# Performance work log

Measured on AMD Instinct MI355X. Metric: run time of the kernel, lower is better.

Reference implementation:

```python
import jax, jax.numpy as jnp
import numpy as np

BS = 256          # batch_size
NN = BS - 1
D = 128           # projection dim
SIGMA = 0.07      # rbf gamma (self.sigma)
C = 1.0
REG = 0.1
NUM_ITERS = 1000
ETA = 0.001
USE_NORM = True


def setup_inputs() -> dict:
    key = jax.random.key(0)
    k1, k2 = jax.random.split(key)
    z = jax.random.normal(k1, (BS, 2, D), dtype=jnp.float32)
    alpha_init = jax.random.normal(k2, (BS, NN, 1), dtype=jnp.float32)
    return {"z": z, "alpha_init": alpha_init}


def _rbf_kernel(X, Y, gamma):
    # exp(-gamma * ||x - y||^2)
    xn = jnp.sum(X * X, axis=1, keepdims=True)          # [n,1]
    yn = jnp.sum(Y * Y, axis=1, keepdims=True).T        # [1,m]
    d = xn + yn - 2.0 * (X @ Y.T)
    return jnp.exp(-gamma * d)


def _pgd_nesterov(DD, p, alpha0, eta, num_iters, C, use_norm):
    # minimize 0.5 a'DDa - p'a  s.t. 0 <= a <= C, batched over bs
    def step(carry, t):
        alpha, alpha_prev = carry
        beta = t / (t + 3.0)
        y = alpha + beta * (alpha - alpha_prev)
        grad = jnp.einsum('bij,bjk->bik', DD, y) - p     # [bs,nn,1]
        if use_norm:
            grad = grad / (jnp.linalg.norm(grad, axis=1, keepdims=True) + 1e-12)
        alpha_new = jnp.clip(y - eta * grad, 0.0, C)
        return (alpha_new, alpha), None
    (alpha, _), _ = jax.lax.scan(step, (alpha0, alpha0),
                                 jnp.arange(num_iters, dtype=jnp.float32))
    return alpha


def reference(z, alpha_init):
    bs, nn = BS, NN
    # F.normalize(z, p=2, dim=1): normalize over the view axis (faithful to source)
    nrm = jnp.maximum(jnp.linalg.norm(z, axis=1, keepdims=True), 1e-12)
    ftr = z / nrm
    ftr = jnp.concatenate([ftr[:, 0, :], ftr[:, 1, :]], axis=0)   # [2bs, d]

    K = _rbf_kernel(ftr[:bs], ftr, SIGMA)                          # [bs, 2bs]

    # ---- QP construction + solve under no_grad ----
    Kd = jax.lax.stop_gradient(K)
    KK = Kd[:, :bs]                                                # block: first bs cols
    r = jnp.arange(bs)
    m = jnp.arange(nn)
    # idx[i] = [0..bs-1] without i  (KMASK row/col removal)
    idx = m[None, :] + (m[None, :] >= r[:, None]).astype(jnp.int32)  # [bs, nn]
    KK_sub = KK[idx[:, :, None], idx[:, None, :]]                  # [bs,nn,nn]
    row = jnp.take_along_axis(KK, idx, axis=1)                     # row[i,m]=KK[i,idx[i,m]]
    # Delta[i,j,k] = 1 + reg*d_jk + KK[j,k] - KK[i,j] - KK[i,k]  (j,k != i)
    DD = (1.0 + REG * jnp.eye(nn, dtype=KK.dtype)[None]
          + KK_sub - row[:, :, None] - row[:, None, :])            # [bs,nn,nn]

    p = 2.0 * jnp.ones((bs, nn, 1), dtype=jnp.float32)
    alpha0 = jnp.clip(jax.nn.relu(alpha_init), 0.0, C)
    alpha = _pgd_nesterov(DD, p, alpha0, ETA, NUM_ITERS, C, USE_NORM)
    alpha_y = jnp.clip(jax.nn.relu(alpha[:, :, 0]), 0.0, C)
    alpha_y = jax.lax.stop_gradient(alpha_y)                       # [bs,nn]
    alpha_x = alpha_y.sum(axis=1)                                  # [bs]

    # ---- loss terms (grad flows through K here) ----
    Ks = K[:, bs:]                                                 # block12: [bs,bs]
    # Kn.T[i,m] = Ks.T[i, idx[i,m]]  (neg_mask = off-diagonal)
    KnT = jnp.take_along_axis(Ks.T, idx, axis=1)                   # [bs,nn]
    pos = jnp.diagonal(Ks)                                         # pos_mask = eye
    pos_loss = jnp.mean(alpha_x * pos)
    neg_loss = jnp.sum(alpha_y * KnT) / bs
    loss = neg_loss - pos_loss

    sparsity = ((alpha_y == C).sum().astype(jnp.float32)
                / ((alpha_y > 0).sum().astype(jnp.float32) + 1e-10))
    num_zero = (alpha_y == 0.0).mean()
    return (loss, pos.mean(), KnT.mean(), sparsity, num_zero, jnp.float32(0.0))
```

## Files before the change

### kernel.cpp

```cpp
#include <hip/hip_runtime.h>
#include <math.h>

#define BS   256
#define NN   255
#define DIM  128
#define GAMMA 0.07
#define NUM_ITERS 1000

typedef float v2f __attribute__((ext_vector_type(2)));

__device__ __forceinline__ double wred_d(double v) {
  #pragma unroll
  for (int k = 1; k < 64; k <<= 1) v += __shfl_xor(v, k, 64);
  return v;
}
__device__ __forceinline__ int wred_i(int v) {
  #pragma unroll
  for (int k = 1; k < 64; k <<= 1) v += __shfl_xor(v, k, 64);
  return v;
}

__device__ __forceinline__ float RLF(float v, int lane) {
  return __int_as_float(__builtin_amdgcn_readlane(__float_as_int(v), lane));
}

template <int CTRL, int RMASK>
__device__ __forceinline__ float dpp_add(float x) {
  int t = __builtin_amdgcn_update_dpp(0, __float_as_int(x), CTRL, RMASK, 0xf, true);
  return x + __int_as_float(t);
}
__device__ __forceinline__ float wred64_dpp(float x) {
  x = dpp_add<0x111, 0xf>(x);
  x = dpp_add<0x112, 0xf>(x);
  x = dpp_add<0x114, 0xf>(x);
  x = dpp_add<0x118, 0xf>(x);
  x = dpp_add<0x142, 0xa>(x);
  x = dpp_add<0x143, 0xc>(x);
  return RLF(x, 63);
}

__device__ __forceinline__ float rsq_nr(float x) {
  float r;
  asm("v_rsq_f32 %0, %1" : "=v"(r) : "v"(x));
  r = r * (1.5f - 0.5f * x * r * r);
  return r;
}

__device__ __forceinline__ void pk_fma(v2f& acc, const v2f& k, const v2f& y) {
  asm("v_pk_fma_f32 %0, %1, %2, %0" : "+v"(acc) : "v"(k), "v"(y));
}

__device__ __forceinline__ v2f pk_add(v2f a, v2f b) {
  v2f d;
  asm("v_pk_add_f32 %0, %1, %2" : "=v"(d) : "v"(a), "v"(b));
  return d;
}

__global__ void k_ftr(const float* __restrict__ z, double* __restrict__ ftrT) {
  int b = blockIdx.x;
  int d = threadIdx.x;
  double z0 = (double)z[b * 256 + d];
  double z1 = (double)z[b * 256 + 128 + d];
  double n = sqrt(z0 * z0 + z1 * z1);
  n = fmax(n, 1e-12);
  ftrT[d * 512 + b]       = z0 / n;
  ftrT[d * 512 + 256 + b] = z1 / n;
}

__global__ void k_K(const double* __restrict__ ftrT, float* __restrict__ K,
                    double* __restrict__ pk_knt, double* __restrict__ pos_arr) {
  int i = blockIdx.x;
  int t = threadIdx.x;
  __shared__ double rowi[DIM];
  __shared__ double redd[4];
  if (t < DIM) rowi[t] = ftrT[t * 512 + i];
  __syncthreads();
  double xn = 0.0;
  #pragma unroll 8
  for (int d = 0; d < DIM; ++d) xn += rowi[d] * rowi[d];

  double knt_part = 0.0;
  #pragma unroll
  for (int h = 0; h < 2; ++h) {
    int j = t + h * 256;
    double dot = 0.0, sq = 0.0;
    #pragma unroll 8
    for (int d = 0; d < DIM; ++d) {
      double f = ftrT[d * 512 + j];
      dot += rowi[d] * f;
      sq  += f * f;
    }
    double dist = xn + sq - 2.0 * dot;
    double kv = exp(-GAMMA * dist);
    K[i * 512 + j] = (float)kv;
    if (h == 1) {
      if (j == 256 + i) pos_arr[i] = kv;
      else knt_part += kv;
    }
  }
  double w = wred_d(knt_part);
  if ((t & 63) == 0) redd[t >> 6] = w;
  __syncthreads();
  if (t == 0) pk_knt[i] = redd[0] + redd[1] + redd[2] + redd[3];
}

__global__ __launch_bounds__(512, 2) void k_pgd(
    const float* __restrict__ K, const float* __restrict__ alpha_init,
    double* __restrict__ neg_arr, double* __restrict__ sa_arr,
    int* __restrict__ cnt1, int* __restrict__ cntp, int* __restrict__ cnt0) {
  int r = blockIdx.x;
  int tid = threadIdx.x;
  int l = tid & 63;
  int rg = tid >> 6;

  __shared__ __align__(16) float ytil[BS];
  __shared__ __align__(16) float part[8][BS];
  __shared__ float betat[1024];

  for (int i = tid; i < 1024; i += 512)
    betat[i] = (float)i / ((float)i + 3.0f);

  v2f kq[64];
  #pragma unroll
  for (int j = 0; j < 16; ++j) {
    float4 r0 = *(const float4*)&K[(32 * rg + 2 * j + 0) * 512 + 4 * l];
    float4 r1 = *(const float4*)&K[(32 * rg + 2 * j + 1) * 512 + 4 * l];
    kq[j].x      = r0.x; kq[j].y      = r1.x;
    kq[16 + j].x = r0.y; kq[16 + j].y = r1.y;
    kq[32 + j].x = r0.z; kq[32 + j].y = r1.z;
    kq[48 + j].x = r0.w; kq[48 + j].y = r1.w;
  }
  #pragma unroll
  for (int j = 0; j < 64; ++j)
    asm volatile("" : "+v"(kq[j]));

  float al[4], ap[4], yv[4], kv[4], rm2[4];
  if (rg == 0) {
    #pragma unroll
    for (int k = 0; k < 4; ++k) {
      int a = 4 * l + k;
      if (a == r) {
        al[k] = 0.f; ap[k] = 0.f; yv[k] = 0.f; kv[k] = 0.f; rm2[k] = 0.f;
      } else {
        int c = a - (a > r ? 1 : 0);
        float v = alpha_init[r * NN + c];
        v = fminf(fmaxf(v, 0.f), 1.f);
        al[k] = v; ap[k] = v; yv[k] = v;
        kv[k] = 1.0f - K[r * 512 + a];
        rm2[k] = 2.0f;
      }
    }
    float4 y4 = {yv[0], yv[1], yv[2], yv[3]};
    *(float4*)&ytil[4 * l] = y4;
  }
  __syncthreads();

  int rq = r >> 2, rc = r & 3;

  for (int it = 0; it < NUM_ITERS; ++it) {
    float beta;
    if (rg == 0) beta = betat[it + 1];

    const float4* yb = (const float4*)&ytil[32 * rg];
    v2f a0 = {0.f, 0.f}, a1 = {0.f, 0.f}, a2 = {0.f, 0.f}, a3 = {0.f, 0.f};
    #pragma unroll
    for (int jj = 0; jj < 8; ++jj) {
      float4 yq = yb[jj];
      v2f ylo = {yq.x, yq.y};
      v2f yhi = {yq.z, yq.w};
      pk_fma(a0, kq[2 * jj],      ylo); pk_fma(a0, kq[2 * jj + 1],      yhi);
      pk_fma(a1, kq[16 + 2 * jj], ylo); pk_fma(a1, kq[16 + 2 * jj + 1], yhi);
      pk_fma(a2, kq[32 + 2 * jj], ylo); pk_fma(a2, kq[32 + 2 * jj + 1], yhi);
      pk_fma(a3, kq[48 + 2 * jj], ylo); pk_fma(a3, kq[48 + 2 * jj + 1], yhi);
    }
    float4 accw = {a0.x + a0.y, a1.x + a1.y, a2.x + a2.y, a3.x + a3.y};

    float Sv;
    if (rg != 0) {
      *(float4*)&part[rg][4 * l] = accw;
    } else {
      Sv = wred64_dpp((yv[0] + yv[1]) + (yv[2] + yv[3]));
    }
    __syncthreads();

    if (rg == 0) {
      v2f q0l = {accw.x, accw.y}, q0h = {accw.z, accw.w};
      float4 q1 = *(const float4*)&part[1][4 * l];
      float4 q2 = *(const float4*)&part[2][4 * l];
      float4 q3 = *(const float4*)&part[3][4 * l];
      float4 q4 = *(const float4*)&part[4][4 * l];
      float4 q5 = *(const float4*)&part[5][4 * l];
      float4 q6 = *(const float4*)&part[6][4 * l];
      float4 q7 = *(const float4*)&part[7][4 * l];
      v2f s01l = pk_add(q0l, (v2f){q1.x, q1.y});
      v2f s01h = pk_add(q0h, (v2f){q1.z, q1.w});
      v2f s23l = pk_add((v2f){q2.x, q2.y}, (v2f){q3.x, q3.y});
      v2f s23h = pk_add((v2f){q2.z, q2.w}, (v2f){q3.z, q3.w});
      v2f s45l = pk_add((v2f){q4.x, q4.y}, (v2f){q5.x, q5.y});
      v2f s45h = pk_add((v2f){q4.z, q4.w}, (v2f){q5.z, q5.w});
      v2f s67l = pk_add((v2f){q6.x, q6.y}, (v2f){q7.x, q7.y});
      v2f s67h = pk_add((v2f){q6.z, q6.w}, (v2f){q7.z, q7.w});
      v2f sAl = pk_add(s01l, s23l);
      v2f sAh = pk_add(s01h, s23h);
      v2f sBl = pk_add(s45l, s67l);
      v2f sBh = pk_add(s45h, s67h);
      v2f gAl = pk_add(sAl, sBl);
      v2f gAh = pk_add(sAh, sBh);
      float4 gA = {gAl.x, gAl.y, gAh.x, gAh.y};
      float grv = (rc == 0) ? gA.x : (rc == 1) ? gA.y : (rc == 2) ? gA.z : gA.w;
      float gr = RLF(grv, rq);
      float g[4];
      g[0] = (gA.x - gr) - rm2[0] + kv[0] * Sv + 0.1f * yv[0];
      g[1] = (gA.y - gr) - rm2[1] + kv[1] * Sv + 0.1f * yv[1];
      g[2] = (gA.z - gr) - rm2[2] + kv[2] * Sv + 0.1f * yv[2];
      g[3] = (gA.w - gr) - rm2[3] + kv[3] * Sv + 0.1f * yv[3];
      float n2 = wred64_dpp((g[0] * g[0] + g[1] * g[1]) + (g[2] * g[2] + g[3] * g[3]));
      float sinv = 0.001f * rsq_nr(n2);
      #pragma unroll
      for (int k = 0; k < 4; ++k) {
        float na = fminf(fmaxf(fmaf(-sinv, g[k], yv[k]), 0.f), 1.f);
        ap[k] = al[k];
        al[k] = na;
        yv[k] = fmaf(beta, na - ap[k], na);
      }
      float4 y4 = {yv[0], yv[1], yv[2], yv[3]};
      *(float4*)&ytil[4 * l] = y4;
    }
    __syncthreads();
  }

  if (rg == 0) {
    double nl = 0.0, sa = 0.0;
    int c1 = 0, cp = 0, cz = 0;
    #pragma unroll
    for (int k = 0; k < 4; ++k) {
      int a = 4 * l + k;
      if (a != r) {
        float kx = K[a * 512 + 256 + r];
        nl += (double)al[k] * (double)kx;
        sa += (double)al[k];
        c1 += (al[k] == 1.0f);
        cp += (al[k] > 0.0f);
        cz += (al[k] == 0.0f);
      }
    }
    nl = wred_d(nl); sa = wred_d(sa);
    c1 = wred_i(c1); cp = wred_i(cp); cz = wred_i(cz);
    if (l == 0) {
      neg_arr[r] = nl;
      sa_arr[r]  = sa;
      cnt1[r] = c1; cntp[r] = cp; cnt0[r] = cz;
    }
  }
}

__global__ void k_fin(const double* __restrict__ pk_knt, const double* __restrict__ pos_arr,
                      const double* __restrict__ neg_arr, const double* __restrict__ sa_arr,
                      const int* __restrict__ cnt1, const int* __restrict__ cntp,
                      const int* __restrict__ cnt0, float* __restrict__ out) {
  int t = threadIdx.x;
  __shared__ double rd[16];
  __shared__ int ri[12];
  double knt = pk_knt[t];
  double pos = pos_arr[t];
  double neg = neg_arr[t];
  double pl  = sa_arr[t] * pos_arr[t];
  int a1 = cnt1[t], ap = cntp[t], a0 = cnt0[t];
  knt = wred_d(knt); pos = wred_d(pos); neg = wred_d(neg); pl = wred_d(pl);
  a1 = wred_i(a1); ap = wred_i(ap); a0 = wred_i(a0);
  int w = t >> 6;
  if ((t & 63) == 0) {
    rd[w] = knt; rd[4 + w] = pos; rd[8 + w] = neg; rd[12 + w] = pl;
    ri[w] = a1; ri[4 + w] = ap; ri[8 + w] = a0;
  }
  __syncthreads();
  if (t == 0) {
    double kntS = rd[0] + rd[1] + rd[2] + rd[3];
    double posS = rd[4] + rd[5] + rd[6] + rd[7];
    double negS = rd[8] + rd[9] + rd[10] + rd[11];
    double plS  = rd[12] + rd[13] + rd[14] + rd[15];
    int c1t = ri[0] + ri[1] + ri[2] + ri[3];
    int cpt = ri[4] + ri[5] + ri[6] + ri[7];
    int c0t = ri[8] + ri[9] + ri[10] + ri[11];
    out[0] = (float)(negS / 256.0 - plS / 256.0);
    out[1] = (float)(posS / 256.0);
    out[2] = (float)(kntS / (256.0 * 255.0));
    out[3] = (float)c1t / ((float)cpt + 1e-10f);
    out[4] = (float)c0t / 65280.0f;
    out[5] = 0.0f;
  }
}

extern "C" void kernel_launch(void* const* d_in, const int* in_sizes, int n_in,
                              void* d_out, int out_size, void* d_ws, size_t ws_size,
                              hipStream_t stream) {
  const float* z     = (const float*)d_in[0];
  const float* ainit = (const float*)d_in[1];
  char* ws = (char*)d_ws;
  double* ftrT   = (double*)ws;
  float*  K      = (float*)(ws + 524288);
  double* pk_knt = (double*)(ws + 1048576);
  double* pos_a  = (double*)(ws + 1048576 + 2048);
  double* neg_a  = (double*)(ws + 1048576 + 4096);
  double* sa_a   = (double*)(ws + 1048576 + 6144);
  int* cnt1 = (int*)(ws + 1048576 + 8192);
  int* cntp = (int*)(ws + 1048576 + 8192 + 1024);
  int* cnt0 = (int*)(ws + 1048576 + 8192 + 2048);
  float* out = (float*)d_out;

  k_ftr<<<256, 128, 0, stream>>>(z, ftrT);
  k_K  <<<256, 256, 0, stream>>>(ftrT, K, pk_knt, pos_a);
  k_pgd<<<256, 512, 0, stream>>>(K, ainit, neg_a, sa_a, cnt1, cntp, cnt0);
  k_fin<<<1, 256, 0, stream>>>(pk_knt, pos_a, neg_a, sa_a, cnt1, cntp, cnt0, out);
}
```

Before: 798.0 us.

## Process two PGD rows per block with interleaved matvec and update phases

Each PGD block now solves two QP rows (A and B) that share the same register-resident K tile. Wave 0 runs row A's serial gradient/norm/update phase while all waves compute row B's matvec, and the reverse in the next half-step. This hides the serial single-wave update latency behind the other row's matvec and halves the grid to 128 blocks. In exchange it doubles the shared-memory buffers and adds register pressure from the two update paths.

```diff
diff --git a/kernel.cpp b/kernel.cpp
--- a/kernel.cpp
+++ b/kernel.cpp
@@ -104,17 +104,84 @@
   if (t == 0) pk_knt[i] = redd[0] + redd[1] + redd[2] + redd[3];
 }
 
+__device__ __forceinline__ float4 matvec8(const v2f* kq, const float* ybase) {
+  const float4* yb = (const float4*)ybase;
+  v2f a0 = {0.f, 0.f}, a1 = {0.f, 0.f}, a2 = {0.f, 0.f}, a3 = {0.f, 0.f};
+  #pragma unroll
+  for (int jj = 0; jj < 8; ++jj) {
+    float4 yq = yb[jj];
+    v2f ylo = {yq.x, yq.y};
+    v2f yhi = {yq.z, yq.w};
+    pk_fma(a0, kq[2 * jj],      ylo); pk_fma(a0, kq[2 * jj + 1],      yhi);
+    pk_fma(a1, kq[16 + 2 * jj], ylo); pk_fma(a1, kq[16 + 2 * jj + 1], yhi);
+    pk_fma(a2, kq[32 + 2 * jj], ylo); pk_fma(a2, kq[32 + 2 * jj + 1], yhi);
+    pk_fma(a3, kq[48 + 2 * jj], ylo); pk_fma(a3, kq[48 + 2 * jj + 1], yhi);
+  }
+  float4 r;
+  r.x = a0.x + a0.y; r.y = a1.x + a1.y; r.z = a2.x + a2.y; r.w = a3.x + a3.y;
+  return r;
+}
+
+template <int OWN>
+__device__ __forceinline__ void phase_b(
+    const float (*part)[BS], const float* qown,
+    float* al, float* ap, float* yv, const float* kv, const float* rm2,
+    int l, int rq, int rc, float beta, float* ytil) {
+  float Sv = wred64_dpp((yv[0] + yv[1]) + (yv[2] + yv[3]));
+  float4 q[8];
+  #pragma unroll
+  for (int m = 0; m < 8; ++m) {
+    if (m == OWN) { q[m].x = qown[0]; q[m].y = qown[1]; q[m].z = qown[2]; q[m].w = qown[3]; }
+    else q[m] = *(const float4*)&part[m][4 * l];
+  }
+  v2f s01l = pk_add((v2f){q[0].x, q[0].y}, (v2f){q[1].x, q[1].y});
+  v2f s01h = pk_add((v2f){q[0].z, q[0].w}, (v2f){q[1].z, q[1].w});
+  v2f s23l = pk_add((v2f){q[2].x, q[2].y}, (v2f){q[3].x, q[3].y});
+  v2f s23h = pk_add((v2f){q[2].z, q[2].w}, (v2f){q[3].z, q[3].w});
+  v2f s45l = pk_add((v2f){q[4].x, q[4].y}, (v2f){q[5].x, q[5].y});
+  v2f s45h = pk_add((v2f){q[4].z, q[4].w}, (v2f){q[5].z, q[5].w});
+  v2f s67l = pk_add((v2f){q[6].x, q[6].y}, (v2f){q[7].x, q[7].y});
+  v2f s67h = pk_add((v2f){q[6].z, q[6].w}, (v2f){q[7].z, q[7].w});
+  v2f sAl = pk_add(s01l, s23l);
+  v2f sAh = pk_add(s01h, s23h);
+  v2f sBl = pk_add(s45l, s67l);
+  v2f sBh = pk_add(s45h, s67h);
+  v2f gAl = pk_add(sAl, sBl);
+  v2f gAh = pk_add(sAh, sBh);
+  float4 gA = {gAl.x, gAl.y, gAh.x, gAh.y};
+  float grv = (rc == 0) ? gA.x : (rc == 1) ? gA.y : (rc == 2) ? gA.z : gA.w;
+  float gr = RLF(grv, rq);
+  float g[4];
+  g[0] = (gA.x - gr) - rm2[0] + kv[0] * Sv + 0.1f * yv[0];
+  g[1] = (gA.y - gr) - rm2[1] + kv[1] * Sv + 0.1f * yv[1];
+  g[2] = (gA.z - gr) - rm2[2] + kv[2] * Sv + 0.1f * yv[2];
+  g[3] = (gA.w - gr) - rm2[3] + kv[3] * Sv + 0.1f * yv[3];
+  float n2 = wred64_dpp((g[0] * g[0] + g[1] * g[1]) + (g[2] * g[2] + g[3] * g[3]));
+  float sinv = 0.001f * rsq_nr(n2);
+  #pragma unroll
+  for (int k = 0; k < 4; ++k) {
+    float na = fminf(fmaxf(fmaf(-sinv, g[k], yv[k]), 0.f), 1.f);
+    ap[k] = al[k];
+    al[k] = na;
+    yv[k] = fmaf(beta, na - ap[k], na);
+  }
+  float4 y4 = {yv[0], yv[1], yv[2], yv[3]};
+  *(float4*)&ytil[4 * l] = y4;
+}
+
 __global__ __launch_bounds__(512, 2) void k_pgd(
     const float* __restrict__ K, const float* __restrict__ alpha_init,
     double* __restrict__ neg_arr, double* __restrict__ sa_arr,
     int* __restrict__ cnt1, int* __restrict__ cntp, int* __restrict__ cnt0) {
-  int r = blockIdx.x;
+  int rA = 2 * blockIdx.x;
+  int rB = 2 * blockIdx.x + 1;
   int tid = threadIdx.x;
   int l = tid & 63;
   int rg = tid >> 6;
 
-  __shared__ __align__(16) float ytil[BS];
-  __shared__ __align__(16) float part[8][BS];
+  __shared__ __align__(16) float ytilA[BS], ytilB[BS];
+  __shared__ __align__(16) float partA[8][BS];
+  __shared__ __align__(16) float partB[8][BS];
   __shared__ float betat[1024];
 
   for (int i = tid; i < 1024; i += 512)
@@ -134,102 +201,66 @@
   for (int j = 0; j < 64; ++j)
     asm volatile("" : "+v"(kq[j]));
 
+  int myr = (rg == 1) ? rB : rA;
   float al[4], ap[4], yv[4], kv[4], rm2[4];
-  if (rg == 0) {
+  if (rg < 2) {
     #pragma unroll
     for (int k = 0; k < 4; ++k) {
       int a = 4 * l + k;
-      if (a == r) {
+      if (a == myr) {
         al[k] = 0.f; ap[k] = 0.f; yv[k] = 0.f; kv[k] = 0.f; rm2[k] = 0.f;
       } else {
-        int c = a - (a > r ? 1 : 0);
-        float v = alpha_init[r * NN + c];
+        int c = a - (a > myr ? 1 : 0);
+        float v = alpha_init[myr * NN + c];
         v = fminf(fmaxf(v, 0.f), 1.f);
         al[k] = v; ap[k] = v; yv[k] = v;
-        kv[k] = 1.0f - K[r * 512 + a];
+        kv[k] = 1.0f - K[myr * 512 + a];
         rm2[k] = 2.0f;
       }
     }
     float4 y4 = {yv[0], yv[1], yv[2], yv[3]};
-    *(float4*)&ytil[4 * l] = y4;
-  }
-  __syncthreads();
-
-  int rq = r >> 2, rc = r & 3;
+    if (rg == 0) *(float4*)&ytilA[4 * l] = y4;
+    else         *(float4*)&ytilB[4 * l] = y4;
+  }
+  __syncthreads();
+
+  int rq = myr >> 2, rc = myr & 3;
+
+  float qown[4];
+
+  {
+    float4 accw = matvec8(kq, &ytilA[32 * rg]);
+    if (rg != 0) *(float4*)&partA[rg][4 * l] = accw;
+    else { qown[0] = accw.x; qown[1] = accw.y; qown[2] = accw.z; qown[3] = accw.w; }
+  }
+  __syncthreads();
 
   for (int it = 0; it < NUM_ITERS; ++it) {
-    float beta;
-    if (rg == 0) beta = betat[it + 1];
-
-    const float4* yb = (const float4*)&ytil[32 * rg];
-    v2f a0 = {0.f, 0.f}, a1 = {0.f, 0.f}, a2 = {0.f, 0.f}, a3 = {0.f, 0.f};
-    #pragma unroll
-    for (int jj = 0; jj < 8; ++jj) {
-      float4 yq = yb[jj];
-      v2f ylo = {yq.x, yq.y};
-      v2f yhi = {yq.z, yq.w};
-      pk_fma(a0, kq[2 * jj],      ylo); pk_fma(a0, kq[2 * jj + 1],      yhi);
-      pk_fma(a1, kq[16 + 2 * jj], ylo); pk_fma(a1, kq[16 + 2 * jj + 1], yhi);
-      pk_fma(a2, kq[32 + 2 * jj], ylo); pk_fma(a2, kq[32 + 2 * jj + 1], yhi);
-      pk_fma(a3, kq[48 + 2 * jj], ylo); pk_fma(a3, kq[48 + 2 * jj + 1], yhi);
-    }
-    float4 accw = {a0.x + a0.y, a1.x + a1.y, a2.x + a2.y, a3.x + a3.y};
-
-    float Sv;
-    if (rg != 0) {
-      *(float4*)&part[rg][4 * l] = accw;
-    } else {
-      Sv = wred64_dpp((yv[0] + yv[1]) + (yv[2] + yv[3]));
+    {
+      float4 accw = matvec8(kq, &ytilB[32 * rg]);
+      if (rg != 1) *(float4*)&partB[rg][4 * l] = accw;
+      else { qown[0] = accw.x; qown[1] = accw.y; qown[2] = accw.z; qown[3] = accw.w; }
+      if (rg == 0) {
+        float beta = betat[it + 1];
+        phase_b<0>(partA, qown, al, ap, yv, kv, rm2, l, rq, rc, beta, ytilA);
+      }
     }
     __syncthreads();
 
-    if (rg == 0) {
-      v2f q0l = {accw.x, accw.y}, q0h = {accw.z, accw.w};
-      float4 q1 = *(const float4*)&part[1][4 * l];
-      float4 q2 = *(const float4*)&part[2][4 * l];
-      float4 q3 = *(const float4*)&part[3][4 * l];
-      float4 q4 = *(const float4*)&part[4][4 * l];
-      float4 q5 = *(const float4*)&part[5][4 * l];
-      float4 q6 = *(const float4*)&part[6][4 * l];
-      float4 q7 = *(const float4*)&part[7][4 * l];
-      v2f s01l = pk_add(q0l, (v2f){q1.x, q1.y});
-      v2f s01h = pk_add(q0h, (v2f){q1.z, q1.w});
-      v2f s23l = pk_add((v2f){q2.x, q2.y}, (v2f){q3.x, q3.y});
-      v2f s23h = pk_add((v2f){q2.z, q2.w}, (v2f){q3.z, q3.w});
-      v2f s45l = pk_add((v2f){q4.x, q4.y}, (v2f){q5.x, q5.y});
-      v2f s45h = pk_add((v2f){q4.z, q4.w}, (v2f){q5.z, q5.w});
-      v2f s67l = pk_add((v2f){q6.x, q6.y}, (v2f){q7.x, q7.y});
-      v2f s67h = pk_add((v2f){q6.z, q6.w}, (v2f){q7.z, q7.w});
-      v2f sAl = pk_add(s01l, s23l);
-      v2f sAh = pk_add(s01h, s23h);
-      v2f sBl = pk_add(s45l, s67l);
-      v2f sBh = pk_add(s45h, s67h);
-      v2f gAl = pk_add(sAl, sBl);
-      v2f gAh = pk_add(sAh, sBh);
-      float4 gA = {gAl.x, gAl.y, gAh.x, gAh.y};
-      float grv = (rc == 0) ? gA.x : (rc == 1) ? gA.y : (rc == 2) ? gA.z : gA.w;
-      float gr = RLF(grv, rq);
-      float g[4];
-      g[0] = (gA.x - gr) - rm2[0] + kv[0] * Sv + 0.1f * yv[0];
-      g[1] = (gA.y - gr) - rm2[1] + kv[1] * Sv + 0.1f * yv[1];
-      g[2] = (gA.z - gr) - rm2[2] + kv[2] * Sv + 0.1f * yv[2];
-      g[3] = (gA.w - gr) - rm2[3] + kv[3] * Sv + 0.1f * yv[3];
-      float n2 = wred64_dpp((g[0] * g[0] + g[1] * g[1]) + (g[2] * g[2] + g[3] * g[3]));
-      float sinv = 0.001f * rsq_nr(n2);
-      #pragma unroll
-      for (int k = 0; k < 4; ++k) {
-        float na = fminf(fmaxf(fmaf(-sinv, g[k], yv[k]), 0.f), 1.f);
-        ap[k] = al[k];
-        al[k] = na;
-        yv[k] = fmaf(beta, na - ap[k], na);
+    {
+      float4 accw = matvec8(kq, &ytilA[32 * rg]);
+      if (rg != 0) *(float4*)&partA[rg][4 * l] = accw;
+      else { qown[0] = accw.x; qown[1] = accw.y; qown[2] = accw.z; qown[3] = accw.w; }
+      if (rg == 1) {
+        float beta = betat[it + 1];
+        phase_b<1>(partB, qown, al, ap, yv, kv, rm2, l, rq, rc, beta, ytilB);
       }
-      float4 y4 = {yv[0], yv[1], yv[2], yv[3]};
-      *(float4*)&ytil[4 * l] = y4;
     }
     __syncthreads();
   }
 
-  if (rg == 0) {
+  if (rg < 2) {
+    int r = myr;
     double nl = 0.0, sa = 0.0;
     int c1 = 0, cp = 0, cz = 0;
     #pragma unroll
@@ -310,6 +341,6 @@
 
   k_ftr<<<256, 128, 0, stream>>>(z, ftrT);
   k_K  <<<256, 256, 0, stream>>>(ftrT, K, pk_knt, pos_a);
-  k_pgd<<<256, 512, 0, stream>>>(K, ainit, neg_a, sa_a, cnt1, cntp, cnt0);
+  k_pgd<<<128, 512, 0, stream>>>(K, ainit, neg_a, sa_a, cnt1, cntp, cnt0);
   k_fin<<<1, 256, 0, stream>>>(pk_knt, pos_a, neg_a, sa_a, cnt1, cntp, cnt0, out);
 }
```

Result: slower. 1.247 ms (+56.3%).
